# Kernel optimization log

Measured on AMD Instinct MI355X. Metric: run time of the kernel, lower is better.

## Reference

```python
import jax, jax.numpy as jnp
import numpy as np

B, N, E = 8, 10000, 320000
IN_DIM, E_H, E_OUT, OUT_DIM = 16, 32, 32, 32
D_EDGE_IN = IN_DIM * 2 + 2 + 1  # src feats + tgt feats + edge_attr_norm(2) + edge_weight(1)


def setup_inputs() -> dict:
    key = jax.random.key(0)
    ks = jax.random.split(key, 10)
    x = jax.random.normal(ks[0], (B, N, IN_DIM), dtype=jnp.float32)
    edge_index = jax.random.randint(ks[1], (2, E), 0, N)
    # col 0 = city_dist (kept >= 0.5 to avoid divide-by-tiny), col 1 = city_direc
    edge_attr = jax.random.uniform(ks[2], (E, 2), dtype=jnp.float32) + 0.5
    wind_mean = jax.random.normal(ks[3], (2,), dtype=jnp.float32)
    wind_std = jax.random.uniform(ks[4], (2,), dtype=jnp.float32) + 0.5
    def lin(k, fo, fi):
        return jax.random.normal(k, (fo, fi), dtype=jnp.float32) / np.sqrt(fi).astype(np.float32)
    W1 = lin(ks[5], E_H, D_EDGE_IN); b1 = jnp.zeros((E_H,), jnp.float32)
    W2 = lin(ks[6], E_OUT, E_H);     b2 = jnp.zeros((E_OUT,), jnp.float32)
    W3 = lin(ks[7], OUT_DIM, E_OUT); b3 = jnp.zeros((OUT_DIM,), jnp.float32)
    return dict(x=x, edge_attr=edge_attr, wind_mean=wind_mean, wind_std=wind_std,
                W1=W1, b1=b1, W2=W2, b2=b2, W3=W3, b3=b3, edge_index=edge_index)


def reference(x, edge_attr, wind_mean, wind_std, W1, b1, W2, b2, W3, b3, edge_index):
    edge_src, edge_tgt = edge_index[0], edge_index[1]
    node_src = x[:, edge_src]   # [B, E, D] gather
    node_tgt = x[:, edge_tgt]   # [B, E, D]
    # de-normalize wind (last two feature channels of source node)
    src_wind = node_src[:, :, -2:] * wind_std[None, None, :] + wind_mean[None, None, :]
    src_wind_speed = src_wind[:, :, 0]
    src_wind_direc = src_wind[:, :, 1]
    city_dist = edge_attr[:, 0][None, :]   # [1, E]
    city_direc = edge_attr[:, 1][None, :]
    theta = jnp.abs(city_direc - src_wind_direc)                       # [B, E]
    edge_weight = jax.nn.relu(3.0 * src_wind_speed * jnp.cos(theta * 360.0 / 16.0) / city_dist)
    # normalization of edge_attr uses torch's unbiased std (ddof=1)
    ea_norm = (edge_attr - edge_attr.mean(axis=0)) / edge_attr.std(axis=0, ddof=1)  # [E, 2]
    feat = jnp.concatenate([
        node_src, node_tgt,
        jnp.broadcast_to(ea_norm[None], (node_src.shape[0], E, 2)),
        edge_weight[:, :, None],
    ], axis=-1)                                                        # [B, E, D_EDGE_IN]
    h = jax.nn.sigmoid(jnp.einsum('bef,hf->beh', feat, W1) + b1)       # edge MLP
    h = jax.nn.sigmoid(jnp.einsum('beh,oh->beo', h, W2) + b2)          # [B, E, E_OUT]
    agg = jnp.zeros((x.shape[0], x.shape[1], h.shape[-1]), h.dtype).at[:, edge_tgt].add(h)
    out = jax.nn.sigmoid(jnp.einsum('bno,po->bnp', agg, W3) + b3)      # node MLP -> [B, N, OUT_DIM]
    return out
```

## Files before the change

kernel.cpp:

```cpp
#include <hip/hip_runtime.h>
#include <hip/hip_fp16.h>
#include <cmath>

constexpr int Bc = 8;
constexpr int Nn = 10000;
constexpr int Ec = 320000;
constexpr int IN = 16;
constexpr int EH = 32;
constexpr int EO = 32;
constexpr int OD = 32;

constexpr float S2 = -1.44269504f;
constexpr float FXS = 65535.0f;

constexpr size_t U_CNT = 8;
constexpr size_t U_CUR = U_CNT + Nn;
constexpr size_t U_REC = 20016;
constexpr size_t U_PA  = U_REC + 4 * (size_t)Ec;
constexpr size_t U_PB  = U_PA + (size_t)Bc * Nn * 16;
constexpr size_t U_PW  = U_PB + (size_t)Bc * Nn * 16;

constexpr int HIST_BLOCKS = 256;
constexpr int PRE_BLOCKS  = (Bc * Nn + 255) / 256;
constexpr int ZERO_BLOCKS = 512;
constexpr int TILES = Ec / 256;

constexpr int WPW = 1408;

typedef _Float16 f16x8 __attribute__((ext_vector_type(8)));
typedef float f32x4 __attribute__((ext_vector_type(4)));

__device__ __forceinline__ float sigmoid_f(float x) {
    return __builtin_amdgcn_rcpf(1.0f + __expf(-x));
}
__device__ __forceinline__ float sig_s(float xs) {
    return __builtin_amdgcn_rcpf(1.0f + __builtin_amdgcn_exp2f(xs));
}
__device__ __forceinline__ unsigned pkh(float lo, float hi) {
    return __builtin_bit_cast(unsigned, __builtin_amdgcn_cvt_pkrtz(lo, hi));
}

__global__ __launch_bounds__(256) void prep_kernel(
    const float* __restrict__ ea, const int* __restrict__ ei,
    const float* __restrict__ x, const float* __restrict__ wmean,
    const float* __restrict__ wstd, const float* __restrict__ W1,
    const float* __restrict__ b1, float* __restrict__ ws,
    float* __restrict__ out)
{
    const int blk = blockIdx.x;
    const int tid = threadIdx.x;

    if (blk < HIST_BLOCKS) {
        int* cnt = (int*)ws + U_CNT;
        const int lo = blk * (Ec / HIST_BLOCKS);
        const int hi = lo + (Ec / HIST_BLOCKS);
        float s0 = 0.f, s1 = 0.f, q0 = 0.f, q1 = 0.f;
        for (int i = lo + tid; i < hi; i += 256) {
            float2 v = reinterpret_cast<const float2*>(ea)[i];
            s0 += v.x; s1 += v.y; q0 += v.x * v.x; q1 += v.y * v.y;
            atomicAdd(&cnt[ei[Ec + i]], 1);
        }
#pragma unroll
        for (int off = 32; off > 0; off >>= 1) {
            s0 += __shfl_down(s0, off);
            s1 += __shfl_down(s1, off);
            q0 += __shfl_down(q0, off);
            q1 += __shfl_down(q1, off);
        }
        if ((tid & 63) == 0) {
            atomicAdd(&ws[0], s0);
            atomicAdd(&ws[1], s1);
            atomicAdd(&ws[2], q0);
            atomicAdd(&ws[3], q1);
        }
    } else if (blk < HIST_BLOCKS + PRE_BLOCKS) {
        const int idx = (blk - HIST_BLOCKS) * 256 + tid;
        if (idx >= Bc * Nn) return;
        const float4* xr = reinterpret_cast<const float4*>(x + (size_t)idx * IN);
        float xv[16];
        float4 t;
        t = xr[0]; xv[0]  = t.x; xv[1]  = t.y; xv[2]  = t.z; xv[3]  = t.w;
        t = xr[1]; xv[4]  = t.x; xv[5]  = t.y; xv[6]  = t.z; xv[7]  = t.w;
        t = xr[2]; xv[8]  = t.x; xv[9]  = t.y; xv[10] = t.z; xv[11] = t.w;
        t = xr[3]; xv[12] = t.x; xv[13] = t.y; xv[14] = t.z; xv[15] = t.w;

        unsigned* PA = (unsigned*)ws + U_PA + (size_t)idx * 16;
        unsigned* PB = (unsigned*)ws + U_PB + (size_t)idx * 16;
#pragma unroll
        for (int p = 0; p < 16; ++p) {
            float a[2], bb[2];
#pragma unroll
            for (int j = 0; j < 2; ++j) {
                const int o = 2 * p + j;
                const float* wr = W1 + o * 35;
                float av = 0.f, bv = b1[o];
#pragma unroll
                for (int f = 0; f < 16; ++f) {
                    av += xv[f] * wr[f];
                    bv += xv[f] * wr[16 + f];
                }
                a[j] = av * S2; bb[j] = bv * S2;
            }
            PA[p] = pkh(a[0], a[1]);
            PB[p] = pkh(bb[0], bb[1]);
        }
        float2* PW = reinterpret_cast<float2*>((unsigned*)ws + U_PW);
        PW[idx] = make_float2(3.0f * (xv[14] * wstd[0] + wmean[0]),
                              xv[15] * wstd[1] + wmean[1]);
    } else {
        float4* o4 = reinterpret_cast<float4*>(out);
        constexpr int TOT4 = Bc * Nn * 32 / 4;
        const float4 z = make_float4(0.f, 0.f, 0.f, 0.f);
        for (int i = (blk - HIST_BLOCKS - PRE_BLOCKS) * 256 + tid; i < TOT4;
             i += ZERO_BLOCKS * 256)
            o4[i] = z;
    }
}

__global__ __launch_bounds__(1024) void scan_kernel(float* __restrict__ ws) {
    const int tid = threadIdx.x;
    const int lane = tid & 63;
    const int w = tid >> 6;
    if (tid == 0) {
        float s0 = ws[0], s1 = ws[1], q0 = ws[2], q1 = ws[3];
        float m0 = s0 / (float)Ec, m1 = s1 / (float)Ec;
        float v0 = (q0 - s0 * m0) / (float)(Ec - 1);
        float v1 = (q1 - s1 * m1) / (float)(Ec - 1);
        const float i0 = S2 * rsqrtf(v0);
        const float i1 = S2 * rsqrtf(v1);
        ws[4] = i0 / FXS; ws[5] = (0.5f - m0) * i0;
        ws[6] = i1 / FXS; ws[7] = (0.5f - m1) * i1;
    }
    int* cnt    = (int*)ws + U_CNT;
    int* cursor = (int*)ws + U_CUR;

    constexpr int PER = 10;
    const int lo = tid * PER;
    int local[PER];
    int sum = 0;
#pragma unroll
    for (int k = 0; k < PER; ++k) {
        const int i = lo + k;
        const int c = (i < Nn) ? cnt[i] : 0;
        local[k] = sum;
        sum += c;
    }
    int v = sum;
#pragma unroll
    for (int off = 1; off < 64; off <<= 1) {
        int u = __shfl_up(v, off);
        if (lane >= off) v += u;
    }
    __shared__ int wt[16];
    __shared__ int woff[16];
    if (lane == 63) wt[w] = v;
    __syncthreads();
    if (w == 0) {
        int t = (lane < 16) ? wt[lane] : 0;
        int tv = t;
#pragma unroll
        for (int off = 1; off < 16; off <<= 1) {
            int u = __shfl_up(tv, off);
            if (lane >= off) tv += u;
        }
        if (lane < 16) woff[lane] = tv - t;
    }
    __syncthreads();
    const int base = woff[w] + (v - sum);
#pragma unroll
    for (int k = 0; k < PER; ++k) {
        const int i = lo + k;
        if (i < Nn) cursor[i] = base + local[k];
    }
}

__global__ __launch_bounds__(256) void record_kernel(const int* __restrict__ ei,
                                                     const float* __restrict__ ea,
                                                     float* __restrict__ ws) {
    int* cursor = (int*)ws + U_CUR;
    uint2* rec  = reinterpret_cast<uint2*>((unsigned*)ws + U_REC);
    const int e = blockIdx.x * 256 + threadIdx.x;
    const int src = ei[e];
    const int tgt = ei[Ec + e];
    const float2 v = reinterpret_cast<const float2*>(ea)[e];
    const unsigned ux = (unsigned)__float2uint_rn((v.x - 0.5f) * FXS);
    const unsigned uy = (unsigned)__float2uint_rn((v.y - 0.5f) * FXS);
    const int pos = atomicAdd(&cursor[tgt], 1);
    rec[pos] = make_uint2((unsigned)src | ((unsigned)tgt << 16), ux | (uy << 16));
}

__global__ __launch_bounds__(256, 7) void edge_kernel(
    const float* __restrict__ W1, const float* __restrict__ W2,
    const float* __restrict__ b2, const float* __restrict__ ws,
    float* __restrict__ agg)
{
    __shared__ unsigned lds[4 * WPW];
    const int tid  = threadIdx.x;
    const int lane = tid & 63;
    const int wid  = tid >> 6;
    unsigned* wl = lds + wid * WPW;

    const int bid = blockIdx.x;
    const int b   = bid & 7;
    const int gid = (bid >> 3) * 256 + wid * 64 + lane;

    const unsigned* wsu = (const unsigned*)ws;
    const uint2 rec = reinterpret_cast<const uint2*>(wsu + U_REC)[gid];
    const int src = (int)(rec.x & 0xFFFFu);
    const int tgt = (int)(rec.x >> 16);
    const float u0 = (float)(rec.y & 0xFFFFu);
    const float u1 = (float)(rec.y >> 16);
    const float eax = fmaf(u0, 1.0f / FXS, 0.5f);
    const float eay = fmaf(u1, 1.0f / FXS, 0.5f);

    const float2 pw = reinterpret_cast<const float2*>(wsu + U_PW)[b * Nn + src];
    const float theta = fabsf(eay - pw.y);
    const float ewtS = fmaxf(pw.x * __cosf(theta * 22.5f) * __builtin_amdgcn_rcpf(eax),
                             0.0f) * S2;
    const float f32v = fmaf(u0, ws[4], ws[5]);
    const float f33v = fmaf(u1, ws[6], ws[7]);

    const uint4* pa4 = reinterpret_cast<const uint4*>(wsu + U_PA + ((size_t)b * Nn + src) * 16);
    const uint4* pb4 = reinterpret_cast<const uint4*>(wsu + U_PB + ((size_t)b * Nn + tgt) * 16);

    unsigned hw[16];
#pragma unroll
    for (int q = 0; q < 4; ++q) {
        const uint4 ua = pa4[q];
        const uint4 ub = pb4[q];
        const unsigned au[4] = {ua.x, ua.y, ua.z, ua.w};
        const unsigned bu[4] = {ub.x, ub.y, ub.z, ub.w};
#pragma unroll
        for (int j = 0; j < 4; ++j) {
            const int p = 4 * q + j;
            const __half2 s = __hadd2(__builtin_bit_cast(__half2, au[j]),
                                      __builtin_bit_cast(__half2, bu[j]));
            const float2 f = __half22float2(s);
            const int o0 = 2 * p, o1 = 2 * p + 1;
            const float acc0 = f.x + f32v * W1[o0 * 35 + 32]
                                   + f33v * W1[o0 * 35 + 33]
                                   + ewtS * W1[o0 * 35 + 34];
            const float acc1 = f.y + f32v * W1[o1 * 35 + 32]
                                   + f33v * W1[o1 * 35 + 33]
                                   + ewtS * W1[o1 * 35 + 34];
            hw[p] = pkh(sig_s(acc0), sig_s(acc1));
        }
    }
    {
        uint4* hrow = reinterpret_cast<uint4*>(wl + lane * 20);
#pragma unroll
        for (int q = 0; q < 4; ++q)
            hrow[q] = make_uint4(hw[4*q], hw[4*q+1], hw[4*q+2], hw[4*q+3]);
    }

    const int tprev = __shfl_up(tgt, 1);
    const bool head = (lane == 0) || (tprev != tgt);
    const unsigned long long mask = __ballot(head);
    const unsigned long long mle = (~0ULL) >> (63 - lane);
    const int run = __popcll(mask & mle) - 1;
    const int nruns = __popcll(mask);
    wl[1280 + lane] = (unsigned)run;
    if (head) wl[1344 + run] = (unsigned)tgt;

    const int c16 = lane & 15;
    const int hq  = lane >> 4;

    f16x8 bw[2];
#pragma unroll
    for (int t = 0; t < 2; ++t) {
        const float* wr = W2 + (c16 + 16 * t) * 32 + 8 * hq;
        const float4 w0 = *reinterpret_cast<const float4*>(wr);
        const float4 w1 = *reinterpret_cast<const float4*>(wr + 4);
        const uint4 pk = make_uint4(pkh(w0.x * S2, w0.y * S2), pkh(w0.z * S2, w0.w * S2),
                                    pkh(w1.x * S2, w1.y * S2), pkh(w1.z * S2, w1.w * S2));
        bw[t] = __builtin_bit_cast(f16x8, pk);
    }

    f32x4 c[4][2];
#pragma unroll
    for (int m = 0; m < 4; ++m) {
        const uint4 av = *reinterpret_cast<const uint4*>(wl + (16 * m + c16) * 20 + 4 * hq);
        const f16x8 afr = __builtin_bit_cast(f16x8, av);
#pragma unroll
        for (int t = 0; t < 2; ++t) {
            f32x4 z = {0.f, 0.f, 0.f, 0.f};
            c[m][t] = __builtin_amdgcn_mfma_f32_16x16x32_f16(afr, bw[t], z, 0, 0, 0);
        }
    }

    __builtin_amdgcn_sched_barrier(0);
    asm volatile("s_waitcnt lgkmcnt(0)" ::: "memory");
    __builtin_amdgcn_sched_barrier(0);

    const float b2v[2] = { b2[c16] * S2, b2[c16 + 16] * S2 };
#pragma unroll
    for (int m = 0; m < 4; ++m) {
#pragma unroll
        for (int t = 0; t < 2; ++t) {
            const float v0 = sig_s(c[m][t][0] + b2v[t]);
            const float v1 = sig_s(c[m][t][1] + b2v[t]);
            const float v2 = sig_s(c[m][t][2] + b2v[t]);
            const float v3 = sig_s(c[m][t][3] + b2v[t]);
            const uint2 pk = make_uint2(pkh(v0, v1), pkh(v2, v3));
            *reinterpret_cast<uint2*>(wl + (c16 + 16 * t) * 36 + 8 * m + 2 * hq) = pk;
        }
    }

    f16x8 vb[2][2];
    unsigned rid[2][8];
#pragma unroll
    for (int kk = 0; kk < 2; ++kk) {
#pragma unroll
        for (int t = 0; t < 2; ++t) {
            const uint4 vv = *reinterpret_cast<const uint4*>(wl + (c16 + 16 * t) * 36 + 16 * kk + 4 * hq);
            vb[kk][t] = __builtin_bit_cast(f16x8, vv);
        }
        const uint4 r0 = *reinterpret_cast<const uint4*>(wl + 1280 + 32 * kk + 8 * hq);
        const uint4 r1 = *reinterpret_cast<const uint4*>(wl + 1280 + 32 * kk + 8 * hq + 4);
        rid[kk][0] = r0.x; rid[kk][1] = r0.y; rid[kk][2] = r0.z; rid[kk][3] = r0.w;
        rid[kk][4] = r1.x; rid[kk][5] = r1.y; rid[kk][6] = r1.z; rid[kk][7] = r1.w;
    }

    const int nm = (nruns + 15) >> 4;
    for (int mr = 0; mr < nm; ++mr) {
        const unsigned rowg = (unsigned)(16 * mr + c16);
        f32x4 d0 = {0.f, 0.f, 0.f, 0.f};
        f32x4 d1 = {0.f, 0.f, 0.f, 0.f};
#pragma unroll
        for (int kk = 0; kk < 2; ++kk) {
            unsigned iw[4];
#pragma unroll
            for (int w = 0; w < 4; ++w) {
                iw[w] = (rid[kk][2 * w]     == rowg ? 0x3C00u : 0u)
                      | (rid[kk][2 * w + 1] == rowg ? 0x3C000000u : 0u);
            }
            const f16x8 ifr = __builtin_bit_cast(f16x8, make_uint4(iw[0], iw[1], iw[2], iw[3]));
            d0 = __builtin_amdgcn_mfma_f32_16x16x32_f16(ifr, vb[kk][0], d0, 0, 0, 0);
            d1 = __builtin_amdgcn_mfma_f32_16x16x32_f16(ifr, vb[kk][1], d1, 0, 0, 0);
        }
#pragma unroll
        for (int r = 0; r < 4; ++r) {
            const int rn = 16 * mr + 4 * hq + r;
            const unsigned tr = wl[1344 + (rn & 63)];
            if (rn < nruns) {
                float* dst = agg + ((size_t)b * Nn + tr) * 32;
                atomicAdd(dst + c16,      d0[r]);
                atomicAdd(dst + c16 + 16, d1[r]);
            }
        }
    }
}

__global__ __launch_bounds__(256) void node_kernel(
    const float* __restrict__ W3, const float* __restrict__ b3,
    float* __restrict__ out)
{
    const int idx = blockIdx.x * 256 + threadIdx.x;
    if (idx >= Bc * Nn) return;
    float* row = out + (size_t)idx * OD;

    float a[EO];
#pragma unroll
    for (int i = 0; i < EO / 4; ++i) {
        float4 t = reinterpret_cast<float4*>(row)[i];
        a[4 * i] = t.x; a[4 * i + 1] = t.y; a[4 * i + 2] = t.z; a[4 * i + 3] = t.w;
    }
    float r[OD];
#pragma unroll
    for (int p = 0; p < OD; ++p) {
        const float* wr = W3 + p * EO;
        float s = b3[p];
#pragma unroll
        for (int o = 0; o < EO; ++o) s += a[o] * wr[o];
        r[p] = sigmoid_f(s);
    }
#pragma unroll
    for (int i = 0; i < OD / 4; ++i) {
        float4 t;
        t.x = r[4 * i + 0]; t.y = r[4 * i + 1];
        t.z = r[4 * i + 2]; t.w = r[4 * i + 3];
        reinterpret_cast<float4*>(row)[i] = t;
    }
}

extern "C" void kernel_launch(void* const* d_in, const int* in_sizes, int n_in,
                              void* d_out, int out_size, void* d_ws, size_t ws_size,
                              hipStream_t stream) {
    const float* x     = (const float*)d_in[0];
    const float* ea    = (const float*)d_in[1];
    const float* wmean = (const float*)d_in[2];
    const float* wstd  = (const float*)d_in[3];
    const float* W1    = (const float*)d_in[4];
    const float* b1    = (const float*)d_in[5];
    const float* W2    = (const float*)d_in[6];
    const float* b2    = (const float*)d_in[7];
    const float* W3    = (const float*)d_in[8];
    const float* b3    = (const float*)d_in[9];
    const int*   ei    = (const int*)d_in[10];
    float* out = (float*)d_out;
    float* ws  = (float*)d_ws;

    hipMemsetAsync(d_ws, 0, (U_CNT + Nn) * sizeof(float), stream);

    prep_kernel<<<HIST_BLOCKS + PRE_BLOCKS + ZERO_BLOCKS, 256, 0, stream>>>(
        ea, ei, x, wmean, wstd, W1, b1, ws, out);
    scan_kernel<<<1, 1024, 0, stream>>>(ws);
    record_kernel<<<Ec / 256, 256, 0, stream>>>(ei, ea, ws);
    edge_kernel<<<TILES * 8, 256, 0, stream>>>(W1, W2, b2, ws, out);
    node_kernel<<<(Bc * Nn + 255) / 256, 256, 0, stream>>>(W3, b3, out);
}
```

Measured before the change: 196.9 us.

## Fuse record pass into edge kernel with grid-wide barrier and persistent tiles

Merges the record (CSR scatter) kernel into the edge kernel. Each block first scatters its share of edge records, then all blocks meet at a global atomic-counter spin barrier, after which a persistent grid of 1280 blocks loops over edge tiles for each batch class. This removes one kernel launch and its inter-kernel gap, and the edge tiles reuse the W2 fragments already held in registers. The cost is a software grid barrier, which needs every block resident at once, plus 64-bit atomic exchanges for record stores, and it depends on memory visibility across CUs.

Result: slower. 286.8 us (+45.7%).

```diff
diff --git a/kernel.cpp b/kernel.cpp
--- a/kernel.cpp
+++ b/kernel.cpp
@@ -13,7 +13,8 @@
 constexpr float S2 = -1.44269504f;
 constexpr float FXS = 65535.0f;
 
-constexpr size_t U_CNT = 8;
+constexpr size_t U_DONE = 8;
+constexpr size_t U_CNT = 9;
 constexpr size_t U_CUR = U_CNT + Nn;
 constexpr size_t U_REC = 20016;
 constexpr size_t U_PA  = U_REC + 4 * (size_t)Ec;
@@ -24,6 +25,7 @@
 constexpr int PRE_BLOCKS  = (Bc * Nn + 255) / 256;
 constexpr int ZERO_BLOCKS = 512;
 constexpr int TILES = Ec / 256;
+constexpr int GRIDB_E = 1280;
 
 constexpr int WPW = 1408;
 
@@ -174,24 +176,10 @@
     }
 }
 
-__global__ __launch_bounds__(256) void record_kernel(const int* __restrict__ ei,
-                                                     const float* __restrict__ ea,
-                                                     float* __restrict__ ws) {
-    int* cursor = (int*)ws + U_CUR;
-    uint2* rec  = reinterpret_cast<uint2*>((unsigned*)ws + U_REC);
-    const int e = blockIdx.x * 256 + threadIdx.x;
-    const int src = ei[e];
-    const int tgt = ei[Ec + e];
-    const float2 v = reinterpret_cast<const float2*>(ea)[e];
-    const unsigned ux = (unsigned)__float2uint_rn((v.x - 0.5f) * FXS);
-    const unsigned uy = (unsigned)__float2uint_rn((v.y - 0.5f) * FXS);
-    const int pos = atomicAdd(&cursor[tgt], 1);
-    rec[pos] = make_uint2((unsigned)src | ((unsigned)tgt << 16), ux | (uy << 16));
-}
-
-__global__ __launch_bounds__(256, 7) void edge_kernel(
+__global__ __launch_bounds__(256, 7) void record_edge_kernel(
+    const int* __restrict__ ei, const float* __restrict__ ea,
     const float* __restrict__ W1, const float* __restrict__ W2,
-    const float* __restrict__ b2, const float* __restrict__ ws,
+    const float* __restrict__ b2, float* __restrict__ ws,
     float* __restrict__ agg)
 {
     __shared__ unsigned lds[4 * WPW];
@@ -199,69 +187,39 @@
     const int lane = tid & 63;
     const int wid  = tid >> 6;
     unsigned* wl = lds + wid * WPW;
-
     const int bid = blockIdx.x;
-    const int b   = bid & 7;
-    const int gid = (bid >> 3) * 256 + wid * 64 + lane;
-
+
+    {
+        const int e = bid * 256 + tid;
+        if (e < Ec) {
+            int* cursor = (int*)ws + U_CUR;
+            unsigned long long* rec =
+                reinterpret_cast<unsigned long long*>((unsigned*)ws + U_REC);
+            const int src = ei[e];
+            const int tgt = ei[Ec + e];
+            const float2 v = reinterpret_cast<const float2*>(ea)[e];
+            const unsigned ux = (unsigned)__float2uint_rn((v.x - 0.5f) * FXS);
+            const unsigned uy = (unsigned)__float2uint_rn((v.y - 0.5f) * FXS);
+            const unsigned lo = (unsigned)src | ((unsigned)tgt << 16);
+            const unsigned hi = ux | (uy << 16);
+            const int pos = atomicAdd(&cursor[tgt], 1);
+            atomicExch(&rec[pos],
+                       (unsigned long long)lo | ((unsigned long long)hi << 32));
+        }
+    }
+
+    __syncthreads();
+    {
+        int* done = (int*)ws + U_DONE;
+        if (tid == 0) {
+            atomicAdd(done, 1);
+            while (atomicAdd(done, 0) < GRIDB_E) __builtin_amdgcn_s_sleep(32);
+        }
+    }
+    __syncthreads();
+
+    const int cls = bid & 7;
     const unsigned* wsu = (const unsigned*)ws;
-    const uint2 rec = reinterpret_cast<const uint2*>(wsu + U_REC)[gid];
-    const int src = (int)(rec.x & 0xFFFFu);
-    const int tgt = (int)(rec.x >> 16);
-    const float u0 = (float)(rec.y & 0xFFFFu);
-    const float u1 = (float)(rec.y >> 16);
-    const float eax = fmaf(u0, 1.0f / FXS, 0.5f);
-    const float eay = fmaf(u1, 1.0f / FXS, 0.5f);
-
-    const float2 pw = reinterpret_cast<const float2*>(wsu + U_PW)[b * Nn + src];
-    const float theta = fabsf(eay - pw.y);
-    const float ewtS = fmaxf(pw.x * __cosf(theta * 22.5f) * __builtin_amdgcn_rcpf(eax),
-                             0.0f) * S2;
-    const float f32v = fmaf(u0, ws[4], ws[5]);
-    const float f33v = fmaf(u1, ws[6], ws[7]);
-
-    const uint4* pa4 = reinterpret_cast<const uint4*>(wsu + U_PA + ((size_t)b * Nn + src) * 16);
-    const uint4* pb4 = reinterpret_cast<const uint4*>(wsu + U_PB + ((size_t)b * Nn + tgt) * 16);
-
-    unsigned hw[16];
-#pragma unroll
-    for (int q = 0; q < 4; ++q) {
-        const uint4 ua = pa4[q];
-        const uint4 ub = pb4[q];
-        const unsigned au[4] = {ua.x, ua.y, ua.z, ua.w};
-        const unsigned bu[4] = {ub.x, ub.y, ub.z, ub.w};
-#pragma unroll
-        for (int j = 0; j < 4; ++j) {
-            const int p = 4 * q + j;
-            const __half2 s = __hadd2(__builtin_bit_cast(__half2, au[j]),
-                                      __builtin_bit_cast(__half2, bu[j]));
-            const float2 f = __half22float2(s);
-            const int o0 = 2 * p, o1 = 2 * p + 1;
-            const float acc0 = f.x + f32v * W1[o0 * 35 + 32]
-                                   + f33v * W1[o0 * 35 + 33]
-                                   + ewtS * W1[o0 * 35 + 34];
-            const float acc1 = f.y + f32v * W1[o1 * 35 + 32]
-                                   + f33v * W1[o1 * 35 + 33]
-                                   + ewtS * W1[o1 * 35 + 34];
-            hw[p] = pkh(sig_s(acc0), sig_s(acc1));
-        }
-    }
-    {
-        uint4* hrow = reinterpret_cast<uint4*>(wl + lane * 20);
-#pragma unroll
-        for (int q = 0; q < 4; ++q)
-            hrow[q] = make_uint4(hw[4*q], hw[4*q+1], hw[4*q+2], hw[4*q+3]);
-    }
-
-    const int tprev = __shfl_up(tgt, 1);
-    const bool head = (lane == 0) || (tprev != tgt);
-    const unsigned long long mask = __ballot(head);
-    const unsigned long long mle = (~0ULL) >> (63 - lane);
-    const int run = __popcll(mask & mle) - 1;
-    const int nruns = __popcll(mask);
-    wl[1280 + lane] = (unsigned)run;
-    if (head) wl[1344 + run] = (unsigned)tgt;
-
     const int c16 = lane & 15;
     const int hq  = lane >> 4;
 
@@ -275,77 +233,142 @@
                                     pkh(w1.x * S2, w1.y * S2), pkh(w1.z * S2, w1.w * S2));
         bw[t] = __builtin_bit_cast(f16x8, pk);
     }
-
-    f32x4 c[4][2];
-#pragma unroll
-    for (int m = 0; m < 4; ++m) {
-        const uint4 av = *reinterpret_cast<const uint4*>(wl + (16 * m + c16) * 20 + 4 * hq);
-        const f16x8 afr = __builtin_bit_cast(f16x8, av);
-#pragma unroll
-        for (int t = 0; t < 2; ++t) {
-            f32x4 z = {0.f, 0.f, 0.f, 0.f};
-            c[m][t] = __builtin_amdgcn_mfma_f32_16x16x32_f16(afr, bw[t], z, 0, 0, 0);
-        }
-    }
-
-    __builtin_amdgcn_sched_barrier(0);
-    asm volatile("s_waitcnt lgkmcnt(0)" ::: "memory");
-    __builtin_amdgcn_sched_barrier(0);
-
     const float b2v[2] = { b2[c16] * S2, b2[c16 + 16] * S2 };
-#pragma unroll
-    for (int m = 0; m < 4; ++m) {
-#pragma unroll
-        for (int t = 0; t < 2; ++t) {
-            const float v0 = sig_s(c[m][t][0] + b2v[t]);
-            const float v1 = sig_s(c[m][t][1] + b2v[t]);
-            const float v2 = sig_s(c[m][t][2] + b2v[t]);
-            const float v3 = sig_s(c[m][t][3] + b2v[t]);
-            const uint2 pk = make_uint2(pkh(v0, v1), pkh(v2, v3));
-            *reinterpret_cast<uint2*>(wl + (c16 + 16 * t) * 36 + 8 * m + 2 * hq) = pk;
-        }
-    }
-
-    f16x8 vb[2][2];
-    unsigned rid[2][8];
-#pragma unroll
-    for (int kk = 0; kk < 2; ++kk) {
-#pragma unroll
-        for (int t = 0; t < 2; ++t) {
-            const uint4 vv = *reinterpret_cast<const uint4*>(wl + (c16 + 16 * t) * 36 + 16 * kk + 4 * hq);
-            vb[kk][t] = __builtin_bit_cast(f16x8, vv);
-        }
-        const uint4 r0 = *reinterpret_cast<const uint4*>(wl + 1280 + 32 * kk + 8 * hq);
-        const uint4 r1 = *reinterpret_cast<const uint4*>(wl + 1280 + 32 * kk + 8 * hq + 4);
-        rid[kk][0] = r0.x; rid[kk][1] = r0.y; rid[kk][2] = r0.z; rid[kk][3] = r0.w;
-        rid[kk][4] = r1.x; rid[kk][5] = r1.y; rid[kk][6] = r1.z; rid[kk][7] = r1.w;
-    }
-
-    const int nm = (nruns + 15) >> 4;
-    for (int mr = 0; mr < nm; ++mr) {
-        const unsigned rowg = (unsigned)(16 * mr + c16);
-        f32x4 d0 = {0.f, 0.f, 0.f, 0.f};
-        f32x4 d1 = {0.f, 0.f, 0.f, 0.f};
+
+#pragma unroll 1
+    for (int tile = bid >> 3; tile < TILES; tile += (GRIDB_E >> 3)) {
+        __builtin_amdgcn_sched_barrier(0);
+        asm volatile("s_waitcnt lgkmcnt(0)" ::: "memory");
+        __builtin_amdgcn_sched_barrier(0);
+
+        const int gid = tile * 256 + wid * 64 + lane;
+        const uint2 rec = reinterpret_cast<const uint2*>(wsu + U_REC)[gid];
+        const int src = (int)(rec.x & 0xFFFFu);
+        const int tgt = (int)(rec.x >> 16);
+        const float u0 = (float)(rec.y & 0xFFFFu);
+        const float u1 = (float)(rec.y >> 16);
+        const float eax = fmaf(u0, 1.0f / FXS, 0.5f);
+        const float eay = fmaf(u1, 1.0f / FXS, 0.5f);
+
+        const float2 pw = reinterpret_cast<const float2*>(wsu + U_PW)[cls * Nn + src];
+        const float theta = fabsf(eay - pw.y);
+        const float ewtS = fmaxf(pw.x * __cosf(theta * 22.5f) * __builtin_amdgcn_rcpf(eax),
+                                 0.0f) * S2;
+        const float f32v = fmaf(u0, ws[4], ws[5]);
+        const float f33v = fmaf(u1, ws[6], ws[7]);
+
+        const uint4* pa4 = reinterpret_cast<const uint4*>(wsu + U_PA + ((size_t)cls * Nn + src) * 16);
+        const uint4* pb4 = reinterpret_cast<const uint4*>(wsu + U_PB + ((size_t)cls * Nn + tgt) * 16);
+
+        unsigned hw[16];
+#pragma unroll
+        for (int q = 0; q < 4; ++q) {
+            const uint4 ua = pa4[q];
+            const uint4 ub = pb4[q];
+            const unsigned au[4] = {ua.x, ua.y, ua.z, ua.w};
+            const unsigned bu[4] = {ub.x, ub.y, ub.z, ub.w};
+#pragma unroll
+            for (int j = 0; j < 4; ++j) {
+                const int p = 4 * q + j;
+                const __half2 s = __hadd2(__builtin_bit_cast(__half2, au[j]),
+                                          __builtin_bit_cast(__half2, bu[j]));
+                const float2 f = __half22float2(s);
+                const int o0 = 2 * p, o1 = 2 * p + 1;
+                const float acc0 = f.x + f32v * W1[o0 * 35 + 32]
+                                       + f33v * W1[o0 * 35 + 33]
+                                       + ewtS * W1[o0 * 35 + 34];
+                const float acc1 = f.y + f32v * W1[o1 * 35 + 32]
+                                       + f33v * W1[o1 * 35 + 33]
+                                       + ewtS * W1[o1 * 35 + 34];
+                hw[p] = pkh(sig_s(acc0), sig_s(acc1));
+            }
+        }
+        {
+            uint4* hrow = reinterpret_cast<uint4*>(wl + lane * 20);
+#pragma unroll
+            for (int q = 0; q < 4; ++q)
+                hrow[q] = make_uint4(hw[4*q], hw[4*q+1], hw[4*q+2], hw[4*q+3]);
+        }
+
+        const int tprev = __shfl_up(tgt, 1);
+        const bool head = (lane == 0) || (tprev != tgt);
+        const unsigned long long mask = __ballot(head);
+        const unsigned long long mle = (~0ULL) >> (63 - lane);
+        const int run = __popcll(mask & mle) - 1;
+        const int nruns = __popcll(mask);
+        wl[1280 + lane] = (unsigned)run;
+        if (head) wl[1344 + run] = (unsigned)tgt;
+
+        f32x4 c[4][2];
+#pragma unroll
+        for (int m = 0; m < 4; ++m) {
+            const uint4 av = *reinterpret_cast<const uint4*>(wl + (16 * m + c16) * 20 + 4 * hq);
+            const f16x8 afr = __builtin_bit_cast(f16x8, av);
+#pragma unroll
+            for (int t = 0; t < 2; ++t) {
+                f32x4 z = {0.f, 0.f, 0.f, 0.f};
+                c[m][t] = __builtin_amdgcn_mfma_f32_16x16x32_f16(afr, bw[t], z, 0, 0, 0);
+            }
+        }
+
+        __builtin_amdgcn_sched_barrier(0);
+        asm volatile("s_waitcnt lgkmcnt(0)" ::: "memory");
+        __builtin_amdgcn_sched_barrier(0);
+
+#pragma unroll
+        for (int m = 0; m < 4; ++m) {
+#pragma unroll
+            for (int t = 0; t < 2; ++t) {
+                const float v0 = sig_s(c[m][t][0] + b2v[t]);
+                const float v1 = sig_s(c[m][t][1] + b2v[t]);
+                const float v2 = sig_s(c[m][t][2] + b2v[t]);
+                const float v3 = sig_s(c[m][t][3] + b2v[t]);
+                const uint2 pk = make_uint2(pkh(v0, v1), pkh(v2, v3));
+                *reinterpret_cast<uint2*>(wl + (c16 + 16 * t) * 36 + 8 * m + 2 * hq) = pk;
+            }
+        }
+
+        f16x8 vb[2][2];
+        unsigned rid[2][8];
 #pragma unroll
         for (int kk = 0; kk < 2; ++kk) {
-            unsigned iw[4];
-#pragma unroll
-            for (int w = 0; w < 4; ++w) {
-                iw[w] = (rid[kk][2 * w]     == rowg ? 0x3C00u : 0u)
-                      | (rid[kk][2 * w + 1] == rowg ? 0x3C000000u : 0u);
-            }
-            const f16x8 ifr = __builtin_bit_cast(f16x8, make_uint4(iw[0], iw[1], iw[2], iw[3]));
-            d0 = __builtin_amdgcn_mfma_f32_16x16x32_f16(ifr, vb[kk][0], d0, 0, 0, 0);
-            d1 = __builtin_amdgcn_mfma_f32_16x16x32_f16(ifr, vb[kk][1], d1, 0, 0, 0);
-        }
-#pragma unroll
-        for (int r = 0; r < 4; ++r) {
-            const int rn = 16 * mr + 4 * hq + r;
-            const unsigned tr = wl[1344 + (rn & 63)];
-            if (rn < nruns) {
-                float* dst = agg + ((size_t)b * Nn + tr) * 32;
-                atomicAdd(dst + c16,      d0[r]);
-                atomicAdd(dst + c16 + 16, d1[r]);
+#pragma unroll
+            for (int t = 0; t < 2; ++t) {
+                const uint4 vv = *reinterpret_cast<const uint4*>(wl + (c16 + 16 * t) * 36 + 16 * kk + 4 * hq);
+                vb[kk][t] = __builtin_bit_cast(f16x8, vv);
+            }
+            const uint4 r0 = *reinterpret_cast<const uint4*>(wl + 1280 + 32 * kk + 8 * hq);
+            const uint4 r1 = *reinterpret_cast<const uint4*>(wl + 1280 + 32 * kk + 8 * hq + 4);
+            rid[kk][0] = r0.x; rid[kk][1] = r0.y; rid[kk][2] = r0.z; rid[kk][3] = r0.w;
+            rid[kk][4] = r1.x; rid[kk][5] = r1.y; rid[kk][6] = r1.z; rid[kk][7] = r1.w;
+        }
+
+        const int nm = (nruns + 15) >> 4;
+        for (int mr = 0; mr < nm; ++mr) {
+            const unsigned rowg = (unsigned)(16 * mr + c16);
+            f32x4 d0 = {0.f, 0.f, 0.f, 0.f};
+            f32x4 d1 = {0.f, 0.f, 0.f, 0.f};
+#pragma unroll
+            for (int kk = 0; kk < 2; ++kk) {
+                unsigned iw[4];
+#pragma unroll
+                for (int w = 0; w < 4; ++w) {
+                    iw[w] = (rid[kk][2 * w]     == rowg ? 0x3C00u : 0u)
+                          | (rid[kk][2 * w + 1] == rowg ? 0x3C000000u : 0u);
+                }
+                const f16x8 ifr = __builtin_bit_cast(f16x8, make_uint4(iw[0], iw[1], iw[2], iw[3]));
+                d0 = __builtin_amdgcn_mfma_f32_16x16x32_f16(ifr, vb[kk][0], d0, 0, 0, 0);
+                d1 = __builtin_amdgcn_mfma_f32_16x16x32_f16(ifr, vb[kk][1], d1, 0, 0, 0);
+            }
+#pragma unroll
+            for (int r = 0; r < 4; ++r) {
+                const int rn = 16 * mr + 4 * hq + r;
+                const unsigned tr = wl[1344 + (rn & 63)];
+                if (rn < nruns) {
+                    float* dst = agg + ((size_t)cls * Nn + tr) * 32;
+                    atomicAdd(dst + c16,      d0[r]);
+                    atomicAdd(dst + c16 + 16, d1[r]);
+                }
             }
         }
     }
@@ -405,7 +428,6 @@
     prep_kernel<<<HIST_BLOCKS + PRE_BLOCKS + ZERO_BLOCKS, 256, 0, stream>>>(
         ea, ei, x, wmean, wstd, W1, b1, ws, out);
     scan_kernel<<<1, 1024, 0, stream>>>(ws);
-    record_kernel<<<Ec / 256, 256, 0, stream>>>(ei, ea, ws);
-    edge_kernel<<<TILES * 8, 256, 0, stream>>>(W1, W2, b2, ws, out);
+    record_edge_kernel<<<GRIDB_E, 256, 0, stream>>>(ei, ea, W1, W2, b2, ws, out);
     node_kernel<<<(Bc * Nn + 255) / 256, 256, 0, stream>>>(W3, b3, out);
 }
```
